# Optimization experiments

Hardware: AMD Instinct MI355X
Metric: run time of the kernel (lower is better)

## Reference

```python
import jax, jax.numpy as jnp
import numpy as np

B, C, H, W = 8, 256, 32, 32
Nh, DK, DV = 8, 64, 64


def conv1x1(x, Wm, b):
    # x: [B,C,H,W], Wm: [O,C] -> [B,O,H,W]
    return jnp.einsum('bchw,oc->bohw', x, Wm) + b[None, :, None, None]


def rel_to_abs(x):
    # x: [B', Nh', L, 2L-1] -> [B', Nh', L, L]
    b, nh, L, _ = x.shape
    x = jnp.pad(x, ((0, 0), (0, 0), (0, 0), (0, 1)))          # [b,nh,L,2L]
    flat = x.reshape(b, nh, L * 2 * L)
    flat = jnp.pad(flat, ((0, 0), (0, 0), (0, L - 1)))
    final = flat.reshape(b, nh, L + 1, 2 * L - 1)
    return final[:, :, :L, L - 1:]


def relative_logits_1d(q, rel_k, Hd, Wd, case):
    # q: [B,Nh,Hd,Wd,dk], rel_k: [2*Wd-1, dk]
    rel = jnp.einsum('bhxyd,md->bhxym', q, rel_k)             # [B,Nh,Hd,Wd,2Wd-1]
    rel = rel.reshape(-1, Nh * Hd, Wd, 2 * Wd - 1)
    rel = rel_to_abs(rel)                                      # [B,Nh*Hd,Wd,Wd]
    rel = rel.reshape(-1, Nh, Hd, Wd, Wd)
    rel = jnp.broadcast_to(rel[:, :, :, None],
                           (rel.shape[0], Nh, Hd, Hd, Wd, Wd))
    if case == 'w':
        rel = rel.transpose((0, 1, 2, 4, 3, 5))                # [B,Nh,H,W,H,W]
    else:  # 'h'
        rel = rel.transpose((0, 1, 4, 2, 5, 3))                # [B,Nh,H,W,H,W]
    return rel.reshape(-1, Nh, Hd * Wd, Hd * Wd)


def setup_inputs() -> dict:
    key = jax.random.key(0)
    ks = jax.random.split(key, 13)
    s = 0.05
    return {
        'q_x': jax.random.normal(ks[0], (B, C, H, W), jnp.float32),
        'k_x': jax.random.normal(ks[1], (B, C, H, W), jnp.float32),
        'v_x': jax.random.normal(ks[2], (B, C, H, W), jnp.float32),
        'Wq': jax.random.normal(ks[3], (Nh * DK, C), jnp.float32) * s,
        'bq': jax.random.normal(ks[4], (Nh * DK,), jnp.float32) * s,
        'Wk': jax.random.normal(ks[5], (Nh * DK, C), jnp.float32) * s,
        'bk': jax.random.normal(ks[6], (Nh * DK,), jnp.float32) * s,
        'Wv': jax.random.normal(ks[7], (Nh * DV, C), jnp.float32) * s,
        'bv': jax.random.normal(ks[8], (Nh * DV,), jnp.float32) * s,
        'Wo': jax.random.normal(ks[9], (DV, Nh * DV), jnp.float32) * s,
        'bo': jax.random.normal(ks[10], (DV,), jnp.float32) * s,
        'key_rel_w': jax.random.normal(ks[11], (2 * W - 1, DK), jnp.float32),
        'key_rel_h': jax.random.normal(ks[12], (2 * H - 1, DK), jnp.float32),
    }


def reference(q_x, k_x, v_x, Wq, bq, Wk, bk, Wv, bv, Wo, bo, key_rel_w, key_rel_h):
    q = conv1x1(q_x, Wq, bq).reshape(B, Nh, DK, H, W) * (DK ** -0.5)
    k = conv1x1(k_x, Wk, bk).reshape(B, Nh, DK, H, W)
    v = conv1x1(v_x, Wv, bv).reshape(B, Nh, DV, H, W)
    flat_q = q.reshape(B, Nh, DK, H * W)
    flat_k = k.reshape(B, Nh, DK, H * W)
    flat_v = v.reshape(B, Nh, DV, H * W)
    # content logits: [B,Nh,HW,HW]
    logits = jnp.einsum('bhdi,bhdj->bhij', flat_q, flat_k)
    # relative logits (Bello et al.)
    qt = q.transpose((0, 1, 3, 4, 2))                          # [B,Nh,H,W,dk]
    w_rel = relative_logits_1d(qt, key_rel_w, H, W, 'w')
    h_rel = relative_logits_1d(qt.transpose((0, 1, 3, 2, 4)), key_rel_h, W, H, 'h')
    logits = logits + h_rel + w_rel
    weights = jax.nn.softmax(logits, axis=-1)
    # [B,Nh,HW,dv] then reshape (NOT transpose) exactly as the torch code does
    attn = jnp.einsum('bhij,bhdj->bhid', weights, flat_v)
    attn = attn.reshape(B, Nh, DV, H, W)
    attn = attn.reshape(B, Nh * DV, H, W)                      # combine heads
    return conv1x1(attn, Wo, bo)                               # [B,dv,H,W]
```

## Files before the change

### kernel.cpp

```cpp
#include <hip/hip_runtime.h>

using f32x4  = __attribute__((ext_vector_type(4))) float;
using f32x16 = __attribute__((ext_vector_type(16))) float;
using bf16x8 = __attribute__((ext_vector_type(8))) short;

__device__ __forceinline__ ushort f2bf(float f) {
  union { float f; unsigned u; } v{f};
  unsigned r = v.u + 0x7FFFu + ((v.u >> 16) & 1u);
  return (ushort)(r >> 16);
}
__device__ __forceinline__ ushort4 f4bf(float4 f) {
  ushort4 r; r.x = f2bf(f.x); r.y = f2bf(f.y); r.z = f2bf(f.z); r.w = f2bf(f.w); return r;
}
__device__ __forceinline__ f32x4 mfma16(bf16x8 a, bf16x8 b, f32x4 c) {
  return __builtin_amdgcn_mfma_f32_16x16x32_bf16(a, b, c, 0, 0, 0);
}
__device__ __forceinline__ f32x16 mfma32(bf16x8 a, bf16x8 b, f32x16 c) {
  return __builtin_amdgcn_mfma_f32_32x32x16_bf16(a, b, c, 0, 0, 0);
}
__device__ __forceinline__ void gload16(const ushort* g, ushort* l) {
  __builtin_amdgcn_global_load_lds(
      (const __attribute__((address_space(1))) void*)g,
      (__attribute__((address_space(3))) void*)l, 16, 0, 0);
}

__global__ __launch_bounds__(256) void prep_all(
    const float* __restrict__ x0, const float* __restrict__ x1,
    const float* __restrict__ x2,
    const float* __restrict__ Wq, const float* __restrict__ Wk,
    const float* __restrict__ Wv, const float* __restrict__ Wo,
    ushort* __restrict__ xT, ushort* __restrict__ Wdst)
{
  __shared__ ushort sT[64 * 72];
  const int bi = blockIdx.x;
  const int t = threadIdx.x;
  if (bi < 1536) {
    const int hw0 = (bi & 15) * 64;
    const int rest = bi >> 4;
    const int y = rest % 12, b = rest / 12;
    const int inp = y >> 2, c0 = (y & 3) * 64;
    const float* src = (inp == 0 ? x0 : inp == 1 ? x1 : x2) +
                       ((size_t)b * 256 + c0) * 1024 + hw0;
    const int clb = t >> 4, hwl = (t & 15) * 4;
#pragma unroll
    for (int cc = 0; cc < 4; ++cc) {
      const int cl = clb + cc * 16;
      const float4 v = *reinterpret_cast<const float4*>(&src[(size_t)cl * 1024 + hwl]);
      *reinterpret_cast<ushort4*>(&sT[cl * 72 + hwl]) = f4bf(v);
    }
    __syncthreads();
    const int hv = t >> 2, cs = (t & 3) * 16;
    ushort tmp[16];
#pragma unroll
    for (int j = 0; j < 16; ++j) tmp[j] = sT[(cs + j) * 72 + hv];
    ushort* dst = xT + (size_t)inp * 2097152 +
                  ((size_t)b * 1024 + hw0 + hv) * 256 + c0 + cs;
    *reinterpret_cast<uint4*>(&dst[0]) = *reinterpret_cast<uint4*>(&tmp[0]);
    *reinterpret_cast<uint4*>(&dst[8]) = *reinterpret_cast<uint4*>(&tmp[8]);
  } else {
    const int idx = ((bi - 1536) * 256 + t) * 8;
    const int r = idx >> 17;
    const float* src = (r == 0 ? Wq : r == 1 ? Wk : r == 2 ? Wv : Wo) + (idx - r * 131072);
    const float4 a = *reinterpret_cast<const float4*>(&src[0]);
    const float4 b = *reinterpret_cast<const float4*>(&src[4]);
    ushort tmp[8];
    *reinterpret_cast<ushort4*>(&tmp[0]) = f4bf(a);
    *reinterpret_cast<ushort4*>(&tmp[4]) = f4bf(b);
    *reinterpret_cast<uint4*>(&Wdst[idx]) = *reinterpret_cast<uint4*>(&tmp[0]);
  }
}

__global__ __launch_bounds__(256) void conv_qkv(
    const ushort* __restrict__ xT, const ushort* __restrict__ WsBf,
    const float* __restrict__ bq, const float* __restrict__ bk,
    const float* __restrict__ bv,
    ushort* __restrict__ outQ, ushort* __restrict__ outK,
    ushort* __restrict__ outV)
{
  __shared__ ushort lds[18432];
  const int z = blockIdx.z, inp = z >> 3, b = z & 7;
  const int t = threadIdx.x, w = t >> 6, lane = t & 63;
  const int li = lane & 15, g = lane >> 4;
  const int o0 = blockIdx.y * 256, hw0 = blockIdx.x * 64;
  const ushort* xb = xT + (size_t)inp * 2097152 + ((size_t)b * 1024 + hw0) * 256;
  const ushort* wb = WsBf + (size_t)inp * 131072 + (size_t)o0 * 256;
  const float* bias = (inp == 0 ? bq : inp == 1 ? bk : bv);
  ushort* out = (inp == 0 ? outQ : inp == 1 ? outK : outV);
  const float scale = (inp == 0) ? 0.125f * 1.44269504f : 1.0f;
  const int MODE = (inp == 2);
  const int srow = t >> 2, sseg = t & 3;

  f32x4 acc[4][4];
#pragma unroll
  for (int i = 0; i < 4; ++i)
#pragma unroll
    for (int j = 0; j < 4; ++j) acc[i][j] = f32x4{0.f, 0.f, 0.f, 0.f};

  for (int ks = 0; ks < 8; ++ks) {
    const int k0 = ks * 32;
    __syncthreads();
    *reinterpret_cast<uint4*>(&lds[srow * 40 + sseg * 8]) =
        *reinterpret_cast<const uint4*>(&xb[(size_t)srow * 256 + k0 + sseg * 8]);
#pragma unroll
    for (int it = 0; it < 4; ++it) {
      const int r = srow + it * 64;
      *reinterpret_cast<uint4*>(&lds[(64 + r) * 40 + sseg * 8]) =
          *reinterpret_cast<const uint4*>(&wb[(size_t)r * 256 + k0 + sseg * 8]);
    }
    __syncthreads();
    bf16x8 af[4], bf[4];
#pragma unroll
    for (int mi = 0; mi < 4; ++mi) {
      const int ra = (!MODE) ? (mi * 16 + li) : (64 + w * 64 + mi * 16 + li);
      af[mi] = *reinterpret_cast<const bf16x8*>(&lds[ra * 40 + g * 8]);
    }
#pragma unroll
    for (int ni = 0; ni < 4; ++ni) {
      const int rb = (!MODE) ? (64 + w * 64 + ni * 16 + li) : (ni * 16 + li);
      bf[ni] = *reinterpret_cast<const bf16x8*>(&lds[rb * 40 + g * 8]);
    }
#pragma unroll
    for (int mi = 0; mi < 4; ++mi)
#pragma unroll
      for (int ni = 0; ni < 4; ++ni)
        acc[mi][ni] = mfma16(af[mi], bf[ni], acc[mi][ni]);
  }
  __syncthreads();

  if (!MODE) {
    float bb[4];
#pragma unroll
    for (int ni = 0; ni < 4; ++ni) bb[ni] = bias[o0 + w * 64 + ni * 16 + li];
#pragma unroll
    for (int mi = 0; mi < 4; ++mi)
#pragma unroll
      for (int ni = 0; ni < 4; ++ni)
#pragma unroll
        for (int r = 0; r < 4; ++r)
          lds[(mi * 16 + g * 4 + r) * 264 + w * 64 + ni * 16 + li] =
              f2bf((acc[mi][ni][r] + bb[ni]) * scale);
    __syncthreads();
    const int row = t & 63;
    ushort* dst = out + (size_t)(b * 8 + (o0 >> 6) + w) * 65536 +
                  (size_t)(hw0 + row) * 64;
#pragma unroll
    for (int seg = 0; seg < 8; ++seg)
      *reinterpret_cast<uint4*>(&dst[seg * 8]) =
          *reinterpret_cast<const uint4*>(&lds[row * 264 + w * 64 + seg * 8]);
  } else {
    const int lis = (li & 3) | ((li & 4) << 1) | ((li & 8) >> 1);
#pragma unroll
    for (int mi = 0; mi < 4; ++mi)
#pragma unroll
      for (int r = 0; r < 4; ++r) {
        const float bb = bias[o0 + w * 64 + mi * 16 + g * 4 + r];
#pragma unroll
        for (int ni = 0; ni < 4; ++ni)
          lds[w * 4608 + (mi * 16 + g * 4 + r) * 72 + ni * 16 + lis] =
              f2bf(acc[mi][ni][r] + bb);
      }
    __syncthreads();
    const int d = t & 63;
    ushort* dst = out + (size_t)(b * 8 + (o0 >> 6) + w) * 65536 +
                  (size_t)d * 1024 + hw0;
#pragma unroll
    for (int seg = 0; seg < 8; ++seg)
      *reinterpret_cast<uint4*>(&dst[seg * 8]) =
          *reinterpret_cast<const uint4*>(&lds[w * 4608 + d * 72 + seg * 8]);
  }
}

__global__ __launch_bounds__(256) void outconv_mfma(
    const float* __restrict__ attnF, const ushort* __restrict__ Wob,
    const float* __restrict__ bias, float* __restrict__ out)
{
  __shared__ float ldsf[64 * 68];
  ushort* lds = reinterpret_cast<ushort*>(ldsf);
  const int t = threadIdx.x, w = t >> 6, lane = t & 63;
  const int li = lane & 15, g = lane >> 4;
  const int b = blockIdx.y, hw0 = blockIdx.x * 64;
  f32x4 acc[4];
#pragma unroll
  for (int i = 0; i < 4; ++i) acc[i] = f32x4{0.f, 0.f, 0.f, 0.f};

  for (int ks = 0; ks < 16; ++ks) {
    const int k0 = ks * 32;
    __syncthreads();
    *reinterpret_cast<uint4*>(&lds[(t >> 2) * 40 + (t & 3) * 8]) =
        *reinterpret_cast<const uint4*>(&Wob[(size_t)(t >> 2) * 512 + k0 + (t & 3) * 8]);
#pragma unroll
    for (int it = 0; it < 2; ++it) {
      const int c = (t >> 4) + it * 16;
      const float4 v = *reinterpret_cast<const float4*>(
          &attnF[((size_t)b * 512 + k0 + c) * 1024 + hw0 + (t & 15) * 4]);
      const int swz = c ^ ((t & 3) << 3);
      const float vv[4] = {v.x, v.y, v.z, v.w};
#pragma unroll
      for (int j = 0; j < 4; ++j)
        lds[2560 + ((t & 15) * 4 + j) * 40 + swz] = f2bf(vv[j]);
    }
    __syncthreads();
    const bf16x8 bfg = *reinterpret_cast<const bf16x8*>(
        &lds[2560 + (w * 16 + li) * 40 + 8 * (g ^ ((li >> 2) & 3))]);
#pragma unroll
    for (int mi = 0; mi < 4; ++mi) {
      const bf16x8 af = *reinterpret_cast<const bf16x8*>(&lds[(mi * 16 + li) * 40 + g * 8]);
      acc[mi] = mfma16(af, bfg, acc[mi]);
    }
  }
  __syncthreads();
#pragma unroll
  for (int mi = 0; mi < 4; ++mi)
#pragma unroll
    for (int r = 0; r < 4; ++r)
      ldsf[(mi * 16 + g * 4 + r) * 68 + w * 16 + li] =
          acc[mi][r] + bias[mi * 16 + g * 4 + r];
  __syncthreads();
  const int o = t >> 2, cs = (t & 3) * 16;
  float* dst = out + ((size_t)b * 64 + o) * 1024 + hw0;
#pragma unroll
  for (int f = 0; f < 4; ++f)
    *reinterpret_cast<float4*>(&dst[cs + f * 4]) =
        *reinterpret_cast<const float4*>(&ldsf[o * 68 + cs + f * 4]);
}

__global__ __launch_bounds__(256, 2) void attn_mfma(
    const ushort* __restrict__ qg, const ushort* __restrict__ kg,
    const ushort* __restrict__ vg, const float* __restrict__ relw,
    const float* __restrict__ relh, float* __restrict__ attn)
{
  __shared__ __align__(16) ushort kv[2][8192];
  __shared__ __align__(16) float tblds[128 * 66];

  const int bn = blockIdx.y;
  const int qb = blockIdx.x * 128;
  const int tid = threadIdx.x;
  const int w = tid >> 6, lane = tid & 63;
  const int li32 = lane & 31, h = lane >> 5;
  const int so = lane & 7;

  const ushort* qbn = qg + (size_t)bn * 65536;
  const ushort* kbn = kg + (size_t)bn * 65536;
  const ushort* vbn = vg + (size_t)bn * 65536;

  const int ldr = lane >> 3;
  auto stage = [&](int cc) {
    const int p = cc & 1;
    if (w < 2) {
#pragma unroll
      for (int inst = 0; inst < 4; ++inst) {
        const int row = w * 32 + inst * 8 + ldr;
        const int col8 = ((lane & 7) ^ (row & 7)) * 8;
        gload16(&kbn[(cc * 64 + row) * 64 + col8],
                &kv[p][(w * 32 + inst * 8) * 64]);
      }
    } else {
#pragma unroll
      for (int inst = 0; inst < 4; ++inst) {
        const int dv = (w - 2) * 32 + inst * 8 + ldr;
        const int col8 = ((lane & 7) ^ (dv & 7)) * 8;
        gload16(&vbn[dv * 1024 + cc * 64 + col8],
                &kv[p][4096 + ((w - 2) * 32 + inst * 8) * 64]);
      }
    }
  };

  stage(0);

  const int qi = qb + w * 32 + li32;
  bf16x8 qf[4];
#pragma unroll
  for (int ks = 0; ks < 4; ++ks)
    qf[ks] = *reinterpret_cast<const bf16x8*>(&qbn[qi * 64 + ks * 16 + 8 * h]);

  float* tb = tblds + (size_t)(w * 32) * 66;
  float rwv[16];
#pragma unroll
  for (int tb2 = 0; tb2 < 2; ++tb2) {
    const float* rel = tb2 ? relh : relw;
#pragma unroll
    for (int mt = 0; mt < 2; ++mt) {
      f32x16 d;
#pragma unroll
      for (int e = 0; e < 16; ++e) d[e] = 0.f;
      const int mm = min(mt * 32 + li32, 62);
#pragma unroll
      for (int ks = 0; ks < 4; ++ks) {
        float tmp[8];
        *reinterpret_cast<float4*>(&tmp[0]) =
            *reinterpret_cast<const float4*>(&rel[mm * 64 + ks * 16 + 8 * h]);
        *reinterpret_cast<float4*>(&tmp[4]) =
            *reinterpret_cast<const float4*>(&rel[mm * 64 + ks * 16 + 8 * h + 4]);
        bf16x8 af;
#pragma unroll
        for (int e = 0; e < 8; ++e) af[e] = (short)f2bf(tmp[e]);
        d = mfma32(af, qf[ks], d);
      }
#pragma unroll
      for (int r = 0; r < 16; ++r)
        tb[li32 * 66 + mt * 32 + ((r & 3) + 8 * (r >> 2) + 4 * h)] = d[r];
    }
    asm volatile("s_waitcnt lgkmcnt(0)" ::: "memory");
    __builtin_amdgcn_sched_barrier(0);
    if (tb2 == 0) {
#pragma unroll
      for (int r = 0; r < 16; ++r)
        rwv[r] = tb[li32 * 65 + ((r & 3) + 8 * (r >> 2) + 4 * h) + 31];
      asm volatile("s_waitcnt lgkmcnt(0)" ::: "memory");
      __builtin_amdgcn_sched_barrier(0);
    }
  }

  const int xq = (qb + w * 32) >> 5;

  f32x16 oacc0, oacc1;
#pragma unroll
  for (int e = 0; e < 16; ++e) { oacc0[e] = 0.f; oacc1[e] = 0.f; }
  float lrun = 0.f;

  for (int c = 0; c < 16; ++c) {
    __syncthreads();
    if (c < 15) stage(c + 1);
    const ushort* Kb = &kv[c & 1][0];
    const ushort* Vb = &kv[c & 1][4096];

    const float2 rhv = *reinterpret_cast<const float2*>(
        &tblds[(w * 32 + li32) * 66 + (c * 2 - xq + 31)]);
    f32x16 s0, s1;
#pragma unroll
    for (int r = 0; r < 16; ++r) { s0[r] = rwv[r] + rhv.x; s1[r] = rwv[r] + rhv.y; }
    __builtin_amdgcn_s_setprio(1);
#pragma unroll
    for (int ks = 0; ks < 4; ++ks) {
      const int oct = ((2 * ks + h) ^ so) * 8;
      const bf16x8 k0 = *reinterpret_cast<const bf16x8*>(&Kb[li32 * 64 + oct]);
      const bf16x8 k1 = *reinterpret_cast<const bf16x8*>(&Kb[(32 + li32) * 64 + oct]);
      s0 = mfma32(k0, qf[ks], s0);
      s1 = mfma32(k1, qf[ks], s1);
    }
    __builtin_amdgcn_s_setprio(0);

    float psum = 0.f;
#pragma unroll
    for (int r = 0; r < 16; ++r) {
      s0[r] = exp2f(s0[r]);
      s1[r] = exp2f(s1[r]);
      psum += s0[r] + s1[r];
    }
    lrun += psum;

    uint pk0[4][2], pk1[4][2];
#pragma unroll
    for (int J = 0; J < 4; ++J) {
      asm("v_cvt_pk_bf16_f32 %0, %1, %2" : "=v"(pk0[J][0]) : "v"(s0[4 * J]), "v"(s0[4 * J + 1]));
      asm("v_cvt_pk_bf16_f32 %0, %1, %2" : "=v"(pk0[J][1]) : "v"(s0[4 * J + 2]), "v"(s0[4 * J + 3]));
      asm("v_cvt_pk_bf16_f32 %0, %1, %2" : "=v"(pk1[J][0]) : "v"(s1[4 * J]), "v"(s1[4 * J + 1]));
      asm("v_cvt_pk_bf16_f32 %0, %1, %2" : "=v"(pk1[J][1]) : "v"(s1[4 * J + 2]), "v"(s1[4 * J + 3]));
    }

    __builtin_amdgcn_s_setprio(1);
#pragma unroll
    for (int ks = 0; ks < 4; ++ks) {
      const int kk = ks & 1;
      uint fu[4];
      if (ks < 2) {
        fu[0] = pk0[2 * kk][0]; fu[1] = pk0[2 * kk][1];
        fu[2] = pk0[2 * kk + 1][0]; fu[3] = pk0[2 * kk + 1][1];
      } else {
        fu[0] = pk1[2 * kk][0]; fu[1] = pk1[2 * kk][1];
        fu[2] = pk1[2 * kk + 1][0]; fu[3] = pk1[2 * kk + 1][1];
      }
      const bf16x8 pa = *reinterpret_cast<const bf16x8*>(&fu[0]);
      const int oct = ((2 * ks + h) ^ so) * 8;
      const bf16x8 v0 = *reinterpret_cast<const bf16x8*>(&Vb[li32 * 64 + oct]);
      const bf16x8 v1 = *reinterpret_cast<const bf16x8*>(&Vb[(32 + li32) * 64 + oct]);
      oacc0 = mfma32(pa, v0, oacc0);
      oacc1 = mfma32(pa, v1, oacc1);
    }
    __builtin_amdgcn_s_setprio(0);
  }

  const float lt = lrun + __shfl_xor(lrun, 32);
  float* ob = attn + (size_t)bn * 65536;
#pragma unroll
  for (int r = 0; r < 16; ++r) {
    const int rp = (r & 3) + 8 * (r >> 2) + 4 * h;
    const float linv = 1.0f / __shfl(lt, rp);
    const size_t qrow = (size_t)(qb + w * 32 + rp) * 64;
    ob[qrow + li32] = oacc0[r] * linv;
    ob[qrow + 32 + li32] = oacc1[r] * linv;
  }
}

extern "C" void kernel_launch(void* const* d_in, const int* in_sizes, int n_in,
                              void* d_out, int out_size, void* d_ws, size_t ws_size,
                              hipStream_t stream) {
  const float* q_x = (const float*)d_in[0];
  const float* k_x = (const float*)d_in[1];
  const float* v_x = (const float*)d_in[2];
  const float* Wq  = (const float*)d_in[3];
  const float* bq  = (const float*)d_in[4];
  const float* Wk  = (const float*)d_in[5];
  const float* bk  = (const float*)d_in[6];
  const float* Wv  = (const float*)d_in[7];
  const float* bv  = (const float*)d_in[8];
  const float* Wo  = (const float*)d_in[9];
  const float* bo  = (const float*)d_in[10];
  const float* krw = (const float*)d_in[11];
  const float* krh = (const float*)d_in[12];

  ushort* wsQ  = (ushort*)d_ws;
  ushort* wsK  = wsQ + 4194304;
  ushort* wsV  = wsK + 4194304;
  ushort* xT   = wsV + 4194304;
  ushort* WsBf = xT + 6291456;
  float*  attnF = (float*)(WsBf + 425984);

  prep_all<<<1744, 256, 0, stream>>>(q_x, k_x, v_x, Wq, Wk, Wv, Wo, xT, WsBf);

  conv_qkv<<<dim3(16, 2, 24), 256, 0, stream>>>(xT, WsBf, bq, bk, bv, wsQ, wsK, wsV);

  attn_mfma<<<dim3(8, 64), 256, 0, stream>>>(wsQ, wsK, wsV, krw, krh, attnF);

  outconv_mfma<<<dim3(16, 8), 256, 0, stream>>>(attnF, WsBf + 393216, bo, (float*)d_out);
}
```

Before: 91.77 us.

## Shrink attention LDS footprint via aliasing and compact rel-h table for occupancy

The attention kernel's separate K/V and relative-table shared buffers are replaced by one packed buffer. The rel-w scratch table now aliases the second K/V stage buffer, and the rel-h logits are stored as a compact per-row 32-entry slice. Launch bounds rise from 2 to 3 blocks per CU. The grid is also flattened so that batch-head varies fastest across block IDs. The aim is to allow more resident blocks per CU, at the cost of a tighter register budget that could cause spills, and with only 512 blocks the extra occupancy may not be used.

```diff
diff --git a/kernel.cpp b/kernel.cpp
--- a/kernel.cpp
+++ b/kernel.cpp
@@ -224,16 +224,20 @@
         *reinterpret_cast<const float4*>(&ldsf[o * 68 + cs + f * 4]);
 }
 
-__global__ __launch_bounds__(256, 2) void attn_mfma(
+__global__ __launch_bounds__(256, 3) void attn_mfma(
     const ushort* __restrict__ qg, const ushort* __restrict__ kg,
     const ushort* __restrict__ vg, const float* __restrict__ relw,
     const float* __restrict__ relh, float* __restrict__ attn)
 {
-  __shared__ __align__(16) ushort kv[2][8192];
-  __shared__ __align__(16) float tblds[128 * 66];
-
-  const int bn = blockIdx.y;
-  const int qb = blockIdx.x * 128;
+  __shared__ __align__(16) unsigned char smem[50176];
+  ushort* kv0 = (ushort*)smem;
+  ushort* kv1 = (ushort*)(smem + 16384);
+  float*  scratch = (float*)(smem + 16384);
+  float*  rhc = (float*)(smem + 32768);
+
+  const int bid = blockIdx.x;
+  const int bn = bid & 63;
+  const int qb = (bid >> 6) * 128;
   const int tid = threadIdx.x;
   const int w = tid >> 6, lane = tid & 63;
   const int li32 = lane & 31, h = lane >> 5;
@@ -245,14 +249,14 @@
 
   const int ldr = lane >> 3;
   auto stage = [&](int cc) {
-    const int p = cc & 1;
+    ushort* dst = (cc & 1) ? kv1 : kv0;
     if (w < 2) {
 #pragma unroll
       for (int inst = 0; inst < 4; ++inst) {
         const int row = w * 32 + inst * 8 + ldr;
         const int col8 = ((lane & 7) ^ (row & 7)) * 8;
         gload16(&kbn[(cc * 64 + row) * 64 + col8],
-                &kv[p][(w * 32 + inst * 8) * 64]);
+                &dst[(w * 32 + inst * 8) * 64]);
       }
     } else {
 #pragma unroll
@@ -260,7 +264,7 @@
         const int dv = (w - 2) * 32 + inst * 8 + ldr;
         const int col8 = ((lane & 7) ^ (dv & 7)) * 8;
         gload16(&vbn[dv * 1024 + cc * 64 + col8],
-                &kv[p][4096 + ((w - 2) * 32 + inst * 8) * 64]);
+                &dst[4096 + ((w - 2) * 32 + inst * 8) * 64]);
       }
     }
   };
@@ -273,45 +277,69 @@
   for (int ks = 0; ks < 4; ++ks)
     qf[ks] = *reinterpret_cast<const bf16x8*>(&qbn[qi * 64 + ks * 16 + 8 * h]);
 
-  float* tb = tblds + (size_t)(w * 32) * 66;
+  const int xq = (qb + w * 32) >> 5;
+
+  float* tbw = scratch + (size_t)(w * 32) * 65;
   float rwv[16];
 #pragma unroll
-  for (int tb2 = 0; tb2 < 2; ++tb2) {
-    const float* rel = tb2 ? relh : relw;
-#pragma unroll
-    for (int mt = 0; mt < 2; ++mt) {
-      f32x16 d;
-#pragma unroll
-      for (int e = 0; e < 16; ++e) d[e] = 0.f;
-      const int mm = min(mt * 32 + li32, 62);
-#pragma unroll
-      for (int ks = 0; ks < 4; ++ks) {
-        float tmp[8];
-        *reinterpret_cast<float4*>(&tmp[0]) =
-            *reinterpret_cast<const float4*>(&rel[mm * 64 + ks * 16 + 8 * h]);
-        *reinterpret_cast<float4*>(&tmp[4]) =
-            *reinterpret_cast<const float4*>(&rel[mm * 64 + ks * 16 + 8 * h + 4]);
-        bf16x8 af;
-#pragma unroll
-        for (int e = 0; e < 8; ++e) af[e] = (short)f2bf(tmp[e]);
-        d = mfma32(af, qf[ks], d);
-      }
-#pragma unroll
-      for (int r = 0; r < 16; ++r)
-        tb[li32 * 66 + mt * 32 + ((r & 3) + 8 * (r >> 2) + 4 * h)] = d[r];
-    }
-    asm volatile("s_waitcnt lgkmcnt(0)" ::: "memory");
-    __builtin_amdgcn_sched_barrier(0);
-    if (tb2 == 0) {
-#pragma unroll
-      for (int r = 0; r < 16; ++r)
-        rwv[r] = tb[li32 * 65 + ((r & 3) + 8 * (r >> 2) + 4 * h) + 31];
-      asm volatile("s_waitcnt lgkmcnt(0)" ::: "memory");
-      __builtin_amdgcn_sched_barrier(0);
-    }
-  }
-
-  const int xq = (qb + w * 32) >> 5;
+  for (int mt = 0; mt < 2; ++mt) {
+    f32x16 d;
+#pragma unroll
+    for (int e = 0; e < 16; ++e) d[e] = 0.f;
+    const int mm = min(mt * 32 + li32, 62);
+#pragma unroll
+    for (int ks = 0; ks < 4; ++ks) {
+      float tmp[8];
+      *reinterpret_cast<float4*>(&tmp[0]) =
+          *reinterpret_cast<const float4*>(&relw[mm * 64 + ks * 16 + 8 * h]);
+      *reinterpret_cast<float4*>(&tmp[4]) =
+          *reinterpret_cast<const float4*>(&relw[mm * 64 + ks * 16 + 8 * h + 4]);
+      bf16x8 af;
+#pragma unroll
+      for (int e = 0; e < 8; ++e) af[e] = (short)f2bf(tmp[e]);
+      d = mfma32(af, qf[ks], d);
+    }
+#pragma unroll
+    for (int r = 0; r < 16; ++r)
+      tbw[li32 * 65 + mt * 32 + ((r & 3) + 8 * (r >> 2) + 4 * h)] = d[r];
+  }
+  asm volatile("s_waitcnt lgkmcnt(0)" ::: "memory");
+  __builtin_amdgcn_sched_barrier(0);
+#pragma unroll
+  for (int r = 0; r < 16; ++r)
+    rwv[r] = tbw[li32 * 64 + ((r & 3) + 8 * (r >> 2) + 4 * h) + 31];
+  asm volatile("s_waitcnt lgkmcnt(0)" ::: "memory");
+  __builtin_amdgcn_sched_barrier(0);
+  __syncthreads();
+
+#pragma unroll
+  for (int mt = 0; mt < 2; ++mt) {
+    f32x16 d;
+#pragma unroll
+    for (int e = 0; e < 16; ++e) d[e] = 0.f;
+    const int mm = min(mt * 32 + li32, 62);
+#pragma unroll
+    for (int ks = 0; ks < 4; ++ks) {
+      float tmp[8];
+      *reinterpret_cast<float4*>(&tmp[0]) =
+          *reinterpret_cast<const float4*>(&relh[mm * 64 + ks * 16 + 8 * h]);
+      *reinterpret_cast<float4*>(&tmp[4]) =
+          *reinterpret_cast<const float4*>(&relh[mm * 64 + ks * 16 + 8 * h + 4]);
+      bf16x8 af;
+#pragma unroll
+      for (int e = 0; e < 8; ++e) af[e] = (short)f2bf(tmp[e]);
+      d = mfma32(af, qf[ks], d);
+    }
+#pragma unroll
+    for (int r = 0; r < 16; ++r) {
+      const int m = mt * 32 + ((r & 3) + 8 * (r >> 2) + 4 * h);
+      const int idx = m - 31 + xq;
+      if ((unsigned)idx < 32u)
+        rhc[(w * 32 + li32) * 34 + idx] = d[r];
+    }
+  }
+  asm volatile("s_waitcnt lgkmcnt(0)" ::: "memory");
+  __builtin_amdgcn_sched_barrier(0);
 
   f32x16 oacc0, oacc1;
 #pragma unroll
@@ -321,11 +349,11 @@
   for (int c = 0; c < 16; ++c) {
     __syncthreads();
     if (c < 15) stage(c + 1);
-    const ushort* Kb = &kv[c & 1][0];
-    const ushort* Vb = &kv[c & 1][4096];
+    const ushort* Kb = (c & 1) ? kv1 : kv0;
+    const ushort* Vb = Kb + 4096;
 
     const float2 rhv = *reinterpret_cast<const float2*>(
-        &tblds[(w * 32 + li32) * 66 + (c * 2 - xq + 31)]);
+        &rhc[(w * 32 + li32) * 34 + 2 * c]);
     f32x16 s0, s1;
 #pragma unroll
     for (int r = 0; r < 16; ++r) { s0[r] = rwv[r] + rhv.x; s1[r] = rwv[r] + rhv.y; }
@@ -420,7 +448,7 @@
 
   conv_qkv<<<dim3(16, 2, 24), 256, 0, stream>>>(xT, WsBf, bq, bk, bv, wsQ, wsK, wsV);
 
-  attn_mfma<<<dim3(8, 64), 256, 0, stream>>>(wsQ, wsK, wsV, krw, krh, attnF);
+  attn_mfma<<<512, 256, 0, stream>>>(wsQ, wsK, wsV, krw, krh, attnF);
 
   outconv_mfma<<<dim3(16, 8), 256, 0, stream>>>(attnF, WsBf + 393216, bo, (float*)d_out);
 }
```

Result: no change. 93.21 us (+1.6%).
